# Optimization experiments

Hardware: AMD Instinct MI355X
Metric: run time of the kernel (lower is better)

## Reference

```python
import jax, jax.numpy as jnp
import numpy as np


def setup_inputs() -> dict:
    key = jax.random.key(0)
    kx, ky = jax.random.split(key)
    x = jax.random.normal(kx, (8, 4096, 3), dtype=jnp.float32)
    y = jax.random.normal(ky, (8, 4096, 3), dtype=jnp.float32)
    return {"x": x, "y": y}


def reference(x, y):
    # Mathematically identical to sum((x[:, :, None] - y[:, None, :])**2, -1)
    # but avoids materializing the [B, n, m, 3] diff tensor.
    x2 = jnp.sum(x * x, axis=-1)              # [B, n]
    y2 = jnp.sum(y * y, axis=-1)              # [B, m]
    xy = jnp.einsum('bnd,bmd->bnm', x, y)     # [B, n, m]
    dist = x2[:, :, None] + y2[:, None, :] - 2.0 * xy  # [B, n, m]
    min_dist_xy = jnp.min(dist, axis=2)       # [B, n] nearest y for each x
    min_dist_yx = jnp.min(dist, axis=1)       # [B, m] nearest x for each y
    return jnp.mean(min_dist_xy, axis=1) + jnp.mean(min_dist_yx, axis=1)  # [B]
```

## Files before the change

### kernel.cpp

```cpp
#include <hip/hip_runtime.h>
#include <math.h>

#define BLK 256
#define NX 8
#define NPTS 4096
#define SLICES 16
#define SLICE 256
#define XT 32
#define XPB 128

__global__ __launch_bounds__(BLK, 2) void chamfer_fused_kernel(
    const float* __restrict__ X, const float* __restrict__ Y,
    float* __restrict__ sums)
{
  __shared__ float4 sh[NPTS];

  int lin = blockIdx.x;
  int xt  = lin & 31; lin >>= 5;
  int b   = lin & 7;
  int dir = lin >> 3;

  const float* xs = (dir ? Y : X) + b * (NPTS * 3);
  const float* ys = (dir ? X : Y) + b * (NPTS * 3);

  int t = threadIdx.x;

  #pragma unroll
  for (int r = 0; r < SLICES; ++r) {
    const float* yp = ys + (r * SLICE + t) * 3;
    float y0 = yp[0], y1 = yp[1], y2 = yp[2];
    sh[r * SLICE + (t ^ (r & 7))] =
        make_float4(y0, y1, y2, 0.5f * (y0 * y0 + y1 * y1 + y2 * y2));
  }

  int x0i = xt * XPB + (t >> 4) * NX;
  float xf[NX * 3];
  {
    const float4* xp = reinterpret_cast<const float4*>(xs + x0i * 3);
    #pragma unroll
    for (int i = 0; i < 6; ++i) {
      float4 p = xp[i];
      xf[i * 4 + 0] = p.x; xf[i * 4 + 1] = p.y;
      xf[i * 4 + 2] = p.z; xf[i * 4 + 3] = p.w;
    }
  }
  float n0[NX], n1[NX], n2[NX], x2h[NX], gm[NX];
  #pragma unroll
  for (int k = 0; k < NX; ++k) {
    float a = xf[k * 3 + 0], bb = xf[k * 3 + 1], cc = xf[k * 3 + 2];
    n0[k] = -a; n1[k] = -bb; n2[k] = -cc;
    x2h[k] = 0.5f * (a * a + bb * bb + cc * cc);
    gm[k] = __builtin_inff();
  }

  __syncthreads();

  int s  = t & 15;
  int mk = s & 7;
  const float4* sp = sh + s * SLICE;
  int o0 = 0 ^ mk, o1 = 1 ^ mk, o2 = 2 ^ mk, o3 = 3 ^ mk;
  int o4 = 4 ^ mk, o5 = 5 ^ mk, o6 = 6 ^ mk, o7 = 7 ^ mk;

  #pragma unroll 2
  for (int w = 0; w < SLICE; w += 8) {
    float4 p0 = sp[w + o0], p1 = sp[w + o1], p2 = sp[w + o2], p3 = sp[w + o3];
    float4 p4 = sp[w + o4], p5 = sp[w + o5], p6 = sp[w + o6], p7 = sp[w + o7];
    #pragma unroll
    for (int k = 0; k < NX; ++k) {
      float g0 = fmaf(n0[k], p0.x, fmaf(n1[k], p0.y, fmaf(n2[k], p0.z, p0.w)));
      float g1 = fmaf(n0[k], p1.x, fmaf(n1[k], p1.y, fmaf(n2[k], p1.z, p1.w)));
      float g2 = fmaf(n0[k], p2.x, fmaf(n1[k], p2.y, fmaf(n2[k], p2.z, p2.w)));
      float g3 = fmaf(n0[k], p3.x, fmaf(n1[k], p3.y, fmaf(n2[k], p3.z, p3.w)));
      float g4 = fmaf(n0[k], p4.x, fmaf(n1[k], p4.y, fmaf(n2[k], p4.z, p4.w)));
      float g5 = fmaf(n0[k], p5.x, fmaf(n1[k], p5.y, fmaf(n2[k], p5.z, p5.w)));
      float g6 = fmaf(n0[k], p6.x, fmaf(n1[k], p6.y, fmaf(n2[k], p6.z, p6.w)));
      float g7 = fmaf(n0[k], p7.x, fmaf(n1[k], p7.y, fmaf(n2[k], p7.z, p7.w)));
      float m0 = fminf(fminf(g0, g1), g2);
      float m1 = fminf(fminf(g3, g4), g5);
      float m2 = fminf(fminf(m0, m1), g6);
      gm[k]    = fminf(fminf(m2, g7), gm[k]);
    }
  }

  #pragma unroll
  for (int mm = 1; mm < 16; mm <<= 1) {
    #pragma unroll
    for (int k = 0; k < NX; ++k)
      gm[k] = fminf(gm[k], __shfl_xor(gm[k], mm, 64));
  }

  float v = 0.0f;
  #pragma unroll
  for (int k = 0; k < NX; ++k) v += 2.0f * (x2h[k] + gm[k]);
  if (s != 0) v = 0.0f;
  #pragma unroll
  for (int mm = 1; mm < 64; mm <<= 1) v += __shfl_xor(v, mm, 64);

  __syncthreads();
  float* red = reinterpret_cast<float*>(sh);
  if ((t & 63) == 0) red[t >> 6] = v;
  __syncthreads();
  if (t == 0) sums[blockIdx.x] = red[0] + red[1] + red[2] + red[3];
}

__global__ __launch_bounds__(512) void chamfer_final_kernel(
    const float* __restrict__ sums, float* __restrict__ out)
{
  __shared__ float gred[16];
  int t = threadIdx.x;
  float v = sums[t];
  #pragma unroll
  for (int mm = 1; mm < 32; mm <<= 1) v += __shfl_xor(v, mm, 64);
  if ((t & 31) == 0) gred[t >> 5] = v;
  __syncthreads();
  if (t < 8) out[t] = (gred[t] + gred[t + 8]) * (1.0f / 4096.0f);
}

__global__ __launch_bounds__(BLK, 2) void chamfer_direct_kernel(
    const float* __restrict__ X, const float* __restrict__ Y,
    float* __restrict__ out)
{
  extern __shared__ float4 shd[];
  int lin = blockIdx.x;
  int xt  = lin & 1;  lin >>= 1;
  int b   = lin & 7;
  int dir = lin >> 3;
  const float* xs = (dir ? Y : X) + b * (NPTS * 3);
  const float* ys = (dir ? X : Y) + b * (NPTS * 3);

  for (int j = threadIdx.x; j < NPTS; j += BLK) {
    float y0 = ys[j * 3 + 0], y1 = ys[j * 3 + 1], y2 = ys[j * 3 + 2];
    shd[j] = make_float4(y0, y1, y2, 0.5f * (y0 * y0 + y1 * y1 + y2 * y2));
  }
  __syncthreads();

  int x0i = xt * (BLK * 8) + threadIdx.x * 8;
  float xf[24];
  const float4* xp = reinterpret_cast<const float4*>(xs + x0i * 3);
  #pragma unroll
  for (int i = 0; i < 6; ++i) {
    float4 p = xp[i];
    xf[i * 4 + 0] = p.x; xf[i * 4 + 1] = p.y;
    xf[i * 4 + 2] = p.z; xf[i * 4 + 3] = p.w;
  }
  float n0[8], n1[8], n2[8], x2h[8], gm[8];
  #pragma unroll
  for (int k = 0; k < 8; ++k) {
    float a = xf[k * 3 + 0], bb = xf[k * 3 + 1], cc = xf[k * 3 + 2];
    n0[k] = -a; n1[k] = -bb; n2[k] = -cc;
    x2h[k] = 0.5f * (a * a + bb * bb + cc * cc);
    gm[k] = __builtin_inff();
  }
  for (int j = 0; j < NPTS; j += 4) {
    float4 p0 = shd[j], p1 = shd[j + 1], p2 = shd[j + 2], p3 = shd[j + 3];
    #pragma unroll
    for (int k = 0; k < 8; ++k) {
      float ga = fmaf(n0[k], p0.x, fmaf(n1[k], p0.y, fmaf(n2[k], p0.z, p0.w)));
      float gb = fmaf(n0[k], p1.x, fmaf(n1[k], p1.y, fmaf(n2[k], p1.z, p1.w)));
      float gc = fmaf(n0[k], p2.x, fmaf(n1[k], p2.y, fmaf(n2[k], p2.z, p2.w)));
      float gd = fmaf(n0[k], p3.x, fmaf(n1[k], p3.y, fmaf(n2[k], p3.z, p3.w)));
      float m  = fminf(fminf(ga, gb), gc);
      gm[k] = fminf(fminf(m, gd), gm[k]);
    }
  }
  float v = 0.0f;
  #pragma unroll
  for (int k = 0; k < 8; ++k) v += 2.0f * (x2h[k] + gm[k]);
  #pragma unroll
  for (int off = 32; off > 0; off >>= 1) v += __shfl_down(v, off, 64);
  __syncthreads();
  float* red = reinterpret_cast<float*>(shd);
  if ((threadIdx.x & 63) == 0) red[threadIdx.x >> 6] = v;
  __syncthreads();
  if (threadIdx.x == 0) {
    float s2 = red[0] + red[1] + red[2] + red[3];
    atomicAdd(&out[b], s2 * (1.0f / 4096.0f));
  }
}

__global__ void zero_out_kernel(float* out)
{
  if (threadIdx.x < 8) out[threadIdx.x] = 0.0f;
}

extern "C" void kernel_launch(void* const* d_in, const int* in_sizes, int n_in,
                              void* d_out, int out_size, void* d_ws, size_t ws_size,
                              hipStream_t stream)
{
  const float* X = (const float*)d_in[0];
  const float* Y = (const float*)d_in[1];
  float* out = (float*)d_out;

  if (ws_size >= (size_t)(2 * 8 * XT) * sizeof(float)) {
    chamfer_fused_kernel<<<2 * 8 * XT, BLK, 0, stream>>>(X, Y, (float*)d_ws);
    chamfer_final_kernel<<<1, 512, 0, stream>>>((const float*)d_ws, out);
  } else {
    zero_out_kernel<<<1, 64, 0, stream>>>(out);
    chamfer_direct_kernel<<<2 * 8 * 2, BLK, NPTS * sizeof(float4), stream>>>(
        X, Y, out);
  }
}
```

Measured before the change: 79.96 us.

## Compute pairwise distances with bf16 MFMA using hi/lo split for fp32 accuracy

```diff
diff --git a/kernel.cpp b/kernel.cpp
--- a/kernel.cpp
+++ b/kernel.cpp
@@ -2,105 +2,140 @@
 #include <math.h>
 
 #define BLK 256
-#define NX 8
 #define NPTS 4096
-#define SLICES 16
-#define SLICE 256
 #define XT 32
-#define XPB 128
-
-__global__ __launch_bounds__(BLK, 2) void chamfer_fused_kernel(
+
+using short8 = __attribute__((ext_vector_type(8))) short;
+using f32x4  = __attribute__((ext_vector_type(4))) float;
+
+__device__ inline unsigned short f2bf(float f) {
+  unsigned u = __float_as_uint(f);
+  return (unsigned short)((u + 0x7FFFu + ((u >> 16) & 1u)) >> 16);
+}
+__device__ inline float bf2f(unsigned short h) {
+  return __uint_as_float((unsigned)h << 16);
+}
+__device__ inline unsigned pk(unsigned short lo, unsigned short hi) {
+  return (unsigned)lo | ((unsigned)hi << 16);
+}
+
+__global__ __launch_bounds__(BLK, 2) void chamfer_mfma_kernel(
     const float* __restrict__ X, const float* __restrict__ Y,
     float* __restrict__ sums)
 {
-  __shared__ float4 sh[NPTS];
-
-  int lin = blockIdx.x;
-  int xt  = lin & 31; lin >>= 5;
-  int b   = lin & 7;
-  int dir = lin >> 3;
+  __shared__ uint4 rec[4096];
+
+  int bid = blockIdx.x;
+  int xt  = bid & 31;
+  int b   = (bid >> 5) & 7;
+  int dir = bid >> 8;
 
   const float* xs = (dir ? Y : X) + b * (NPTS * 3);
   const float* ys = (dir ? X : Y) + b * (NPTS * 3);
 
   int t = threadIdx.x;
-
-  #pragma unroll
-  for (int r = 0; r < SLICES; ++r) {
-    const float* yp = ys + (r * SLICE + t) * 3;
-    float y0 = yp[0], y1 = yp[1], y2 = yp[2];
-    sh[r * SLICE + (t ^ (r & 7))] =
-        make_float4(y0, y1, y2, 0.5f * (y0 * y0 + y1 * y1 + y2 * y2));
-  }
-
-  int x0i = xt * XPB + (t >> 4) * NX;
-  float xf[NX * 3];
+  int lane = t & 63;
+  int w = t >> 6;
+  int g = lane >> 4;
+  int c = lane & 15;
+
+  int xbase = xt * 128 + w * 32;
+  const float* xpa = xs + (xbase + c) * 3;
+  const float* xpb = xs + (xbase + 16 + c) * 3;
+  float xa0 = xpa[0], xa1 = xpa[1], xa2 = xpa[2];
+  float xb0 = xpb[0], xb1 = xpb[1], xb2 = xpb[2];
+  float x2a = fmaf(xa0, xa0, fmaf(xa1, xa1, xa2 * xa2));
+  float x2b = fmaf(xb0, xb0, fmaf(xb1, xb1, xb2 * xb2));
+
+  const unsigned short ONE = 0x3F80;
+  short8 b0f = (short8)0, b1f = (short8)0;
   {
-    const float4* xp = reinterpret_cast<const float4*>(xs + x0i * 3);
+    unsigned short ha0 = f2bf(xa0), ha1 = f2bf(xa1), ha2 = f2bf(xa2);
+    unsigned short la0 = f2bf(xa0 - bf2f(ha0));
+    unsigned short la1 = f2bf(xa1 - bf2f(ha1));
+    unsigned short la2 = f2bf(xa2 - bf2f(ha2));
+    unsigned short hb0 = f2bf(xb0), hb1 = f2bf(xb1), hb2 = f2bf(xb2);
+    unsigned short lb0 = f2bf(xb0 - bf2f(hb0));
+    unsigned short lb1 = f2bf(xb1 - bf2f(hb1));
+    unsigned short lb2 = f2bf(xb2 - bf2f(hb2));
+    unsigned short mha0 = f2bf(-2.0f * bf2f(ha0));
+    unsigned short mha1 = f2bf(-2.0f * bf2f(ha1));
+    unsigned short mha2 = f2bf(-2.0f * bf2f(ha2));
+    unsigned short mla0 = f2bf(-2.0f * bf2f(la0));
+    unsigned short mla1 = f2bf(-2.0f * bf2f(la1));
+    unsigned short mla2 = f2bf(-2.0f * bf2f(la2));
+    unsigned short mhb0 = f2bf(-2.0f * bf2f(hb0));
+    unsigned short mhb1 = f2bf(-2.0f * bf2f(hb1));
+    unsigned short mhb2 = f2bf(-2.0f * bf2f(hb2));
+    unsigned short mlb0 = f2bf(-2.0f * bf2f(lb0));
+    unsigned short mlb1 = f2bf(-2.0f * bf2f(lb1));
+    unsigned short mlb2 = f2bf(-2.0f * bf2f(lb2));
+    if (g == 0) {
+      b0f[0] = mha0; b0f[1] = mha1; b0f[2] = mha2; b0f[3] = mha0;
+      b0f[4] = mha1; b0f[5] = mha2; b0f[6] = mla0; b0f[7] = mla1;
+      b1f[0] = mhb0; b1f[1] = mhb1; b1f[2] = mhb2; b1f[3] = mhb0;
+      b1f[4] = mhb1; b1f[5] = mhb2; b1f[6] = mlb0; b1f[7] = mlb1;
+    } else if (g == 1) {
+      b0f[0] = mla2; b0f[1] = mla0; b0f[2] = mla1; b0f[3] = mla2;
+      b0f[4] = ONE;  b0f[5] = ONE;  b0f[6] = ONE;  b0f[7] = 0;
+      b1f[0] = mlb2; b1f[1] = mlb0; b1f[2] = mlb1; b1f[3] = mlb2;
+      b1f[4] = ONE;  b1f[5] = ONE;  b1f[6] = ONE;  b1f[7] = 0;
+    }
+  }
+
+  float gm0 = __builtin_inff(), gm1 = __builtin_inff();
+  f32x4 cz = {0.0f, 0.0f, 0.0f, 0.0f};
+  const short8* recp = reinterpret_cast<const short8*>(rec);
+  int aoff = (g & 1) * 2048 + c;
+
+  for (int p = 0; p < 2; ++p) {
     #pragma unroll
-    for (int i = 0; i < 6; ++i) {
-      float4 p = xp[i];
-      xf[i * 4 + 0] = p.x; xf[i * 4 + 1] = p.y;
-      xf[i * 4 + 2] = p.z; xf[i * 4 + 3] = p.w;
-    }
-  }
-  float n0[NX], n1[NX], n2[NX], x2h[NX], gm[NX];
-  #pragma unroll
-  for (int k = 0; k < NX; ++k) {
-    float a = xf[k * 3 + 0], bb = xf[k * 3 + 1], cc = xf[k * 3 + 2];
-    n0[k] = -a; n1[k] = -bb; n2[k] = -cc;
-    x2h[k] = 0.5f * (a * a + bb * bb + cc * cc);
-    gm[k] = __builtin_inff();
-  }
-
-  __syncthreads();
-
-  int s  = t & 15;
-  int mk = s & 7;
-  const float4* sp = sh + s * SLICE;
-  int o0 = 0 ^ mk, o1 = 1 ^ mk, o2 = 2 ^ mk, o3 = 3 ^ mk;
-  int o4 = 4 ^ mk, o5 = 5 ^ mk, o6 = 6 ^ mk, o7 = 7 ^ mk;
-
-  #pragma unroll 2
-  for (int w = 0; w < SLICE; w += 8) {
-    float4 p0 = sp[w + o0], p1 = sp[w + o1], p2 = sp[w + o2], p3 = sp[w + o3];
-    float4 p4 = sp[w + o4], p5 = sp[w + o5], p6 = sp[w + o6], p7 = sp[w + o7];
-    #pragma unroll
-    for (int k = 0; k < NX; ++k) {
-      float g0 = fmaf(n0[k], p0.x, fmaf(n1[k], p0.y, fmaf(n2[k], p0.z, p0.w)));
-      float g1 = fmaf(n0[k], p1.x, fmaf(n1[k], p1.y, fmaf(n2[k], p1.z, p1.w)));
-      float g2 = fmaf(n0[k], p2.x, fmaf(n1[k], p2.y, fmaf(n2[k], p2.z, p2.w)));
-      float g3 = fmaf(n0[k], p3.x, fmaf(n1[k], p3.y, fmaf(n2[k], p3.z, p3.w)));
-      float g4 = fmaf(n0[k], p4.x, fmaf(n1[k], p4.y, fmaf(n2[k], p4.z, p4.w)));
-      float g5 = fmaf(n0[k], p5.x, fmaf(n1[k], p5.y, fmaf(n2[k], p5.z, p5.w)));
-      float g6 = fmaf(n0[k], p6.x, fmaf(n1[k], p6.y, fmaf(n2[k], p6.z, p6.w)));
-      float g7 = fmaf(n0[k], p7.x, fmaf(n1[k], p7.y, fmaf(n2[k], p7.z, p7.w)));
-      float m0 = fminf(fminf(g0, g1), g2);
-      float m1 = fminf(fminf(g3, g4), g5);
-      float m2 = fminf(fminf(m0, m1), g6);
-      gm[k]    = fminf(fminf(m2, g7), gm[k]);
-    }
-  }
-
-  #pragma unroll
-  for (int mm = 1; mm < 16; mm <<= 1) {
-    #pragma unroll
-    for (int k = 0; k < NX; ++k)
-      gm[k] = fminf(gm[k], __shfl_xor(gm[k], mm, 64));
-  }
-
-  float v = 0.0f;
-  #pragma unroll
-  for (int k = 0; k < NX; ++k) v += 2.0f * (x2h[k] + gm[k]);
-  if (s != 0) v = 0.0f;
+    for (int i = 0; i < 8; ++i) {
+      int yl_ = t + i * 256;
+      const float* yp = ys + (p * 2048 + yl_) * 3;
+      float y0 = yp[0], y1 = yp[1], y2c = yp[2];
+      unsigned short h0 = f2bf(y0), h1 = f2bf(y1), h2 = f2bf(y2c);
+      unsigned short l0 = f2bf(y0 - bf2f(h0));
+      unsigned short l1 = f2bf(y1 - bf2f(h1));
+      unsigned short l2 = f2bf(y2c - bf2f(h2));
+      float ysq = fmaf(y0, y0, fmaf(y1, y1, y2c * y2c));
+      unsigned short s0 = f2bf(ysq);
+      float r1 = ysq - bf2f(s0);
+      unsigned short s1 = f2bf(r1);
+      unsigned short s2 = f2bf(r1 - bf2f(s1));
+      uint4 w0, w1;
+      w0.x = pk(h0, h1); w0.y = pk(h2, l0); w0.z = pk(l1, l2); w0.w = pk(h0, h1);
+      w1.x = pk(h2, l0); w1.y = pk(l1, l2); w1.z = pk(s0, s1); w1.w = pk(s2, 0);
+      rec[yl_] = w0;
+      rec[2048 + yl_] = w1;
+    }
+    __syncthreads();
+
+    #pragma unroll 4
+    for (int tile = 0; tile < 128; ++tile) {
+      short8 a = recp[aoff + tile * 16];
+      f32x4 d0 = __builtin_amdgcn_mfma_f32_16x16x32_bf16(a, b0f, cz, 0, 0, 0);
+      f32x4 d1 = __builtin_amdgcn_mfma_f32_16x16x32_bf16(a, b1f, cz, 0, 0, 0);
+      float m0 = fminf(fminf(d0[0], d0[1]), d0[2]);
+      gm0 = fminf(fminf(m0, d0[3]), gm0);
+      float m1 = fminf(fminf(d1[0], d1[1]), d1[2]);
+      gm1 = fminf(fminf(m1, d1[3]), gm1);
+    }
+    __syncthreads();
+  }
+
+  gm0 = fminf(gm0, __shfl_xor(gm0, 16, 64));
+  gm0 = fminf(gm0, __shfl_xor(gm0, 32, 64));
+  gm1 = fminf(gm1, __shfl_xor(gm1, 16, 64));
+  gm1 = fminf(gm1, __shfl_xor(gm1, 32, 64));
+  float v = (lane < 16) ? (gm0 + x2a) + (gm1 + x2b) : 0.0f;
   #pragma unroll
   for (int mm = 1; mm < 64; mm <<= 1) v += __shfl_xor(v, mm, 64);
 
-  __syncthreads();
-  float* red = reinterpret_cast<float*>(sh);
-  if ((t & 63) == 0) red[t >> 6] = v;
-  __syncthreads();
-  if (t == 0) sums[blockIdx.x] = red[0] + red[1] + red[2] + red[3];
+  float* red = reinterpret_cast<float*>(rec);
+  if (lane == 0) red[w] = v;
+  __syncthreads();
+  if (t == 0) sums[bid] = (red[0] + red[1]) + (red[2] + red[3]);
 }
 
 __global__ __launch_bounds__(512) void chamfer_final_kernel(
@@ -192,7 +227,7 @@
   float* out = (float*)d_out;
 
   if (ws_size >= (size_t)(2 * 8 * XT) * sizeof(float)) {
-    chamfer_fused_kernel<<<2 * 8 * XT, BLK, 0, stream>>>(X, Y, (float*)d_ws);
+    chamfer_mfma_kernel<<<2 * 8 * XT, BLK, 0, stream>>>(X, Y, (float*)d_ws);
     chamfer_final_kernel<<<1, 512, 0, stream>>>((const float*)d_ws, out);
   } else {
     zero_out_kernel<<<1, 64, 0, stream>>>(out);
```

Result: faster. 70.88 us (-11.4%).
